# Optimization experiments

Hardware: AMD Instinct MI355X
Metric: run time of the kernel (lower is better)

## Reference

```python
import jax, jax.numpy as jnp
import numpy as np

N_NODES = 50000
N_EDGES = 800000
FEAT_SIZE = 4096
EMB = 30          # embedding_size
HID = 80          # hidden_size
VOCAB = 10
HEADS = 2
TEMP = 1.0
GAT_SLOPE = 0.2   # DGL GATConv leaky_relu negative_slope
CONV_SLOPE = 0.01 # torch LeakyReLU default


def _lrelu(x, s):
    return jnp.where(x >= 0, x, s * x)


def gat_layer(feat, W, al, ar, b, src, dst, n_nodes):
    """DGL GATConv: feat [N, ..., Fin] -> [N, ..., H, Fout].
    W: [Fin, H*Fout]; al, ar, b: [H, Fout]."""
    H, F = al.shape
    z = jnp.tensordot(feat, W, axes=1).reshape(feat.shape[:-1] + (H, F))  # [N,...,H,F]
    el = (z * al).sum(-1, keepdims=True)  # [N,...,H,1]
    er = (z * ar).sum(-1, keepdims=True)
    e = _lrelu(el[src] + er[dst], GAT_SLOPE)            # [E,...,H,1]
    emax = jax.ops.segment_max(e, dst, num_segments=n_nodes)
    ex = jnp.exp(e - emax[dst])
    denom = jax.ops.segment_sum(ex, dst, num_segments=n_nodes)
    alpha = ex / denom[dst]                              # edge softmax per dst
    rst = jax.ops.segment_sum(z[src] * alpha, dst, num_segments=n_nodes)
    return rst + b


def setup_inputs() -> dict:
    key = jax.random.key(0)
    ks = jax.random.split(key, 24)
    s = 0.1
    return {
        "x": jax.random.normal(ks[0], (2, FEAT_SIZE), jnp.float32),
        "vocab": jax.random.normal(ks[1], (VOCAB,), jnp.float32),
        "node_feats": jax.random.normal(ks[2], (2, N_NODES, 3), jnp.float32),
        "src": jax.random.randint(ks[3], (2, N_EDGES), 0, N_NODES, jnp.int32),
        "dst": jax.random.randint(ks[4], (2, N_EDGES), 0, N_NODES, jnp.int32),
        "W_lin1": jax.random.normal(ks[5], (FEAT_SIZE, EMB), jnp.float32) * s,
        "Wc1": jax.random.normal(ks[6], (HID, 2), jnp.float32) * s,
        "Wc2": jax.random.normal(ks[7], (HID,), jnp.float32) * s,
        "gat1_W": jax.random.normal(ks[8], (3, HEADS * HID), jnp.float32) * s,
        "gat1_al": jax.random.normal(ks[9], (HEADS, HID), jnp.float32) * s,
        "gat1_ar": jax.random.normal(ks[10], (HEADS, HID), jnp.float32) * s,
        "gat1_b": jax.random.normal(ks[11], (HEADS, HID), jnp.float32) * s,
        "gat2_W": jax.random.normal(ks[12], (HID, HEADS * EMB), jnp.float32) * s,
        "gat2_al": jax.random.normal(ks[13], (HEADS, EMB), jnp.float32) * s,
        "gat2_ar": jax.random.normal(ks[14], (HEADS, EMB), jnp.float32) * s,
        "gat2_b": jax.random.normal(ks[15], (HEADS, EMB), jnp.float32) * s,
        "Wg1": jax.random.normal(ks[16], (2 * EMB, EMB), jnp.float32) * s,
        "bg1": jax.random.normal(ks[17], (EMB,), jnp.float32) * s,
        "W2": jax.random.normal(ks[18], (2 * EMB + VOCAB, HID), jnp.float32) * s,
        "W3": jax.random.normal(ks[19], (HID, 2), jnp.float32) * s,
    }


def reference(x, vocab, node_feats, src, dst, W_lin1, Wc1, Wc2,
              gat1_W, gat1_al, gat1_ar, gat1_b,
              gat2_W, gat2_al, gat2_ar, gat2_b,
              Wg1, bg1, W2, W3):
    # deterministic order = [0, 1] (original shuffles); order.index(0) == 0
    # image branch: per-game embedding -> [2, EMB]
    emb = x @ W_lin1                          # [2, EMB]
    h = _lrelu(Wc1 @ emb, CONV_SLOPE)         # im_conv1: [HID, EMB]
    h = _lrelu(Wc2 @ h, CONV_SLOPE)           # im_conv2: [EMB]
    # graph branch: two GAT layers per graph, mean over nodes, take head 0
    gr_emb = []
    for i in range(2):
        g1 = gat_layer(node_feats[i], gat1_W, gat1_al, gat1_ar, gat1_b,
                       src[i], dst[i], N_NODES)          # [N, H, HID]
        g1 = jax.nn.relu(g1)
        g2 = gat_layer(g1, gat2_W, gat2_al, gat2_ar, gat2_b,
                       src[i], dst[i], N_NODES)          # [N, H, H, EMB]
        a = g2.mean(axis=0)[0, 0]                        # mean_nodes then a[0][0][0] -> [EMB]
        gr_emb.append(a)
    gr = jnp.concatenate(gr_emb) @ Wg1 + bg1             # [EMB]
    hc = jnp.concatenate([gr, h, vocab])                 # [2*EMB + VOCAB]
    logits = jax.nn.log_softmax(((hc @ W2) @ W3) * (1.0 / TEMP), axis=0)
    return logits, 0
```

## Files before the change

### kernel.cpp

```cpp
#include <hip/hip_runtime.h>
#include <math.h>

#define NN 50000
#define NE 800000

#define CH 196
#define C  256
#define CAP 3600
#define BSL 2048

__device__ __forceinline__ float lrelu(float x, float s) { return x >= 0.f ? x : s * x; }

__global__ void k_pre(const float* __restrict__ x, const float* __restrict__ Wl,
                      const float* __restrict__ nodef,
                      const float* __restrict__ W1, const float* __restrict__ al1,
                      const float* __restrict__ ar1,
                      const int* __restrict__ src, const int* __restrict__ dst,
                      float* __restrict__ imgp, float* __restrict__ feat4,
                      float* __restrict__ er1, unsigned* __restrict__ gctr,
                      unsigned* __restrict__ dbin, unsigned* __restrict__ sbin) {
    int bid = blockIdx.x, t = threadIdx.x;
    if (bid < 64) {
        __shared__ float part[8][64];
        int kk = t & 31, rq = t >> 5;
        int r0 = bid * 64;
        float a0 = 0.f, a1 = 0.f;
        if (kk < 30) {
            for (int i = 0; i < 8; ++i) {
                int r = r0 + rq * 8 + i;
                float wv = Wl[r * 30 + kk];
                a0 += x[r] * wv;
                a1 += x[4096 + r] * wv;
            }
        }
        part[rq][kk] = a0;
        part[rq][32 + kk] = a1;
        __syncthreads();
        if (t < 60) {
            int g = t / 30, k = t - g * 30;
            float s = 0.f;
            #pragma unroll
            for (int rr = 0; rr < 8; ++rr) s += part[rr][g * 32 + k];
            imgp[bid * 64 + g * 32 + k] = s;
        }
    } else if (bid < 456) {
        __shared__ float sP[6];
        if (t < 6) {
            int c = t >> 1;
            const float* av = (t & 1) ? ar1 : al1;
            float s = 0.f;
            for (int f = 0; f < 80; ++f) s += W1[c * 160 + f] * av[f];
            sP[(t & 1) * 3 + c] = s;
        }
        __syncthreads();
        int b2 = bid - 64;
        int g = b2 / 196;
        int n = (b2 - g * 196) * 256 + t;
        if (n < NN) {
            const float* f = nodef + ((size_t)g * NN + n) * 3;
            float f0 = f[0], f1 = f[1], f2 = f[2];
            *(float4*)(feat4 + ((size_t)g * NN + n) * 4) =
                make_float4(f0, f1, f2, f0 * sP[0] + f1 * sP[1] + f2 * sP[2]);
            er1[g * NN + n] = f0 * sP[3] + f1 * sP[4] + f2 * sP[5];
        }
    } else {
        __shared__ unsigned wcnt[4][C];
        __shared__ unsigned wbase[4][C];
        __shared__ unsigned wrun[4][C];
        __shared__ unsigned sbase2[C];
        int b3 = bid - 456;
        int a = b3 / 782;
        int rem2 = b3 - a * 782;
        int g = rem2 / 391;
        int bx = rem2 - g * 391;
        int wid = t >> 6;
        for (int i = t; i < 4 * C; i += 256) ((unsigned*)wcnt)[i] = 0;
        __syncthreads();
        const int* ip = (a ? src : dst) + (size_t)g * NE;
        const int* pp = (a ? dst : src) + (size_t)g * NE;
        unsigned* bin = (a ? sbin : dbin);
        int cbase = (a * 2 + g) * C;
        int bbase = g * C;
        int e0 = bx * BSL + t * 8;
        int nv = 0;
        if (e0 < NE) nv = (NE - e0) < 8 ? (NE - e0) : 8;
        unsigned cj[8], pk[8];
        if (nv == 8) {
            int4 v0 = *(const int4*)(ip + e0), v1 = *(const int4*)(ip + e0 + 4);
            int4 q0 = *(const int4*)(pp + e0), q1 = *(const int4*)(pp + e0 + 4);
            int dj[8] = {v0.x, v0.y, v0.z, v0.w, v1.x, v1.y, v1.z, v1.w};
            int pj[8] = {q0.x, q0.y, q0.z, q0.w, q1.x, q1.y, q1.z, q1.w};
            #pragma unroll
            for (int j = 0; j < 8; ++j) {
                unsigned c = (unsigned)dj[j] / CH;
                cj[j] = c;
                pk[j] = (((unsigned)dj[j] - c * CH) << 16) | (unsigned)pj[j];
                atomicAdd(&wcnt[wid][c], 1u);
            }
        } else {
            for (int j = 0; j < nv; ++j) {
                int dv = ip[e0 + j], pv = pp[e0 + j];
                unsigned c = (unsigned)dv / CH;
                cj[j] = c;
                pk[j] = (((unsigned)dv - c * CH) << 16) | (unsigned)pv;
                atomicAdd(&wcnt[wid][c], 1u);
            }
        }
        __syncthreads();
        if (t < C) {
            unsigned s = wcnt[0][t] + wcnt[1][t] + wcnt[2][t] + wcnt[3][t];
            sbase2[t] = atomicAdd(&gctr[cbase + t], s);
        }
        __syncthreads();
        for (int i = t; i < 4 * C; i += 256) {
            int w2 = i / C, b = i - w2 * C;
            unsigned off2 = 0;
            for (int w3 = 0; w3 < w2; ++w3) off2 += wcnt[w3][b];
            wbase[w2][b] = sbase2[b] + off2;
            wrun[w2][b] = 0;
        }
        __syncthreads();
        for (int j = 0; j < nv; ++j) {
            unsigned c = cj[j];
            unsigned slot = atomicAdd(&wrun[wid][c], 1u);
            unsigned pos = wbase[wid][c] + slot;
            if (pos < CAP) bin[(size_t)(bbase + c) * CAP + pos] = pk[j];
        }
    }
}

__global__ __launch_bounds__(1024) void k_e1n(const unsigned* __restrict__ dbin,
                                              const unsigned* __restrict__ gctr,
                                              const float* __restrict__ feat4,
                                              const float* __restrict__ er1,
                                              const float* __restrict__ W1,
                                              const float* __restrict__ b1,
                                              const float* __restrict__ W2,
                                              const float* __restrict__ al2,
                                              const float* __restrict__ ar2,
                                              float* __restrict__ facc4,
                                              float* __restrict__ el2,
                                              float* __restrict__ er2iv) {
    __shared__ unsigned scnt[CH];
    __shared__ unsigned sstart[CH + 1];
    __shared__ unsigned sofs[CH];
    __shared__ unsigned ssort[CAP];
    __shared__ float sEr[CH];
    __shared__ float pacc[8][CH];
    __shared__ float sW[240], sB[80], sU[80], sV[80];
    int c = blockIdx.x, g = blockIdx.y, t = threadIdx.x;
    int base = c * CH;
    if (t < CH) {
        scnt[t] = 0;
        sEr[t] = (base + t < NN) ? er1[(size_t)g * NN + base + t] : 0.f;
    }
    if (t >= 1024 - 80) {
        int f = t - (1024 - 80);
        sW[f] = W1[f];
        sW[80 + f] = W1[160 + f];
        sW[160 + f] = W1[320 + f];
        sB[f] = b1[f];
        float u = 0.f, v = 0.f;
        for (int j = 0; j < 30; ++j) {
            float wv = W2[f * 60 + j];
            u += wv * al2[j];
            v += wv * ar2[j];
        }
        sU[f] = u;
        sV[f] = v;
    }
    __syncthreads();
    const unsigned* seg = dbin + (size_t)(g * C + c) * CAP;
    unsigned size = gctr[g * C + c];
    if (size > CAP) size = CAP;
    for (unsigned i = t; i < size; i += 1024) atomicAdd(&scnt[seg[i] >> 16], 1u);
    __syncthreads();
    if (t == 0) {
        unsigned run = 0;
        for (int j = 0; j < CH; ++j) { sstart[j] = run; run += scnt[j]; }
        sstart[CH] = run;
    }
    __syncthreads();
    if (t < CH) sofs[t] = sstart[t];
    __syncthreads();
    for (unsigned i = t; i < size; i += 1024) {
        unsigned p = seg[i];
        unsigned slot = atomicAdd(&sofs[p >> 16], 1u);
        ssort[slot] = p & 0xFFFFu;
    }
    __syncthreads();
    const float* f4 = feat4 + (size_t)g * NN * 4;
    if (t < 2 * CH) {
        int rel = t >> 1, half = t & 1;
        unsigned start = sstart[rel], end = sstart[rel + 1];
        unsigned mid = (start + end) >> 1;
        unsigned lo = half ? mid : start;
        unsigned hi = half ? end : mid;
        float ax = 0.f, ay = 0.f, az = 0.f, aw = 0.f;
        float erv = sEr[rel];
        for (unsigned j = lo; j < hi; ++j) {
            unsigned s = ssort[j];
            float4 F = *(const float4*)(f4 + (size_t)s * 4);
            float wv = __expf(lrelu(F.w + erv, 0.2f));
            ax += wv * F.x; ay += wv * F.y; az += wv * F.z; aw += wv;
        }
        int hb = half * 4;
        pacc[hb + 0][rel] = ax;
        pacc[hb + 1][rel] = ay;
        pacc[hb + 2][rel] = az;
        pacc[hb + 3][rel] = aw;
    }
    __syncthreads();
    if (t < CH && base + t < NN) {
        size_t n = (size_t)g * NN + base + t;
        float fx = pacc[0][t] + pacc[4][t];
        float fy = pacc[1][t] + pacc[5][t];
        float fz = pacc[2][t] + pacc[6][t];
        float fw = pacc[3][t] + pacc[7][t];
        *(float4*)(facc4 + n * 4) = make_float4(fx, fy, fz, fw);
        float inv = fw != 0.f ? 1.f / fw : 0.f;
        float c0 = fx * inv, c1 = fy * inv, c2 = fz * inv;
        float el = 0.f, er = 0.f;
        #pragma unroll
        for (int f = 0; f < 80; ++f) {
            float gg = c0 * sW[f] + c1 * sW[80 + f] + c2 * sW[160 + f] + sB[f];
            gg = gg > 0.f ? gg : 0.f;
            el += gg * sU[f];
            er += gg * sV[f];
        }
        el2[n] = el;
        er2iv[n * 2] = er;
    }
}

__global__ __launch_bounds__(1024) void k_e2d(const unsigned* __restrict__ dbin,
                                              const unsigned* __restrict__ gctr,
                                              const float* __restrict__ el2,
                                              float* __restrict__ er2iv) {
    __shared__ float sden[CH], sEr2[CH];
    int c = blockIdx.x, g = blockIdx.y, t = threadIdx.x;
    int base = c * CH;
    if (t < CH) {
        sden[t] = 0.f;
        sEr2[t] = (base + t < NN) ? er2iv[((size_t)g * NN + base + t) * 2] : 0.f;
    }
    __syncthreads();
    const float* el = el2 + (size_t)g * NN;
    const unsigned* seg = dbin + (size_t)(g * C + c) * CAP;
    unsigned size = gctr[g * C + c];
    if (size > CAP) size = CAP;
    for (unsigned i = t; i < size; i += 1024) {
        unsigned p = seg[i];
        unsigned rel = p >> 16;
        atomicAdd(&sden[rel], __expf(lrelu(el[p & 0xFFFFu] + sEr2[rel], 0.2f)));
    }
    __syncthreads();
    if (t < CH && base + t < NN) {
        float s = sden[t];
        er2iv[((size_t)g * NN + base + t) * 2 + 1] = s != 0.f ? 1.f / s : 0.f;
    }
}

__global__ __launch_bounds__(1024) void k_e3q(const unsigned* __restrict__ sbin,
                                              const unsigned* __restrict__ gctr,
                                              const float* __restrict__ el2,
                                              const float* __restrict__ er2iv,
                                              const float* __restrict__ facc4,
                                              const float* __restrict__ W1,
                                              const float* __restrict__ b1,
                                              float* __restrict__ Apart) {
    __shared__ float sq[CH], sEl[CH];
    __shared__ float cx[CH], cy[CH], cz[CH];
    __shared__ float pacc2[12][80];
    __shared__ float sW[240], sB[80];
    int c = blockIdx.x, g = blockIdx.y, t = threadIdx.x;
    int base = c * CH;
    if (t < CH) {
        sq[t] = 0.f;
        sEl[t] = (base + t < NN) ? el2[(size_t)g * NN + base + t] : 0.f;
    }
    if (t >= 1024 - 80) {
        int f = t - (1024 - 80);
        sW[f] = W1[f];
        sW[80 + f] = W1[160 + f];
        sW[160 + f] = W1[320 + f];
        sB[f] = b1[f];
    }
    __syncthreads();
    const float* er = er2iv + (size_t)g * NN * 2;
    const unsigned* seg = sbin + (size_t)(g * C + c) * CAP;
    unsigned size = gctr[(2 + g) * C + c];
    if (size > CAP) size = CAP;
    for (unsigned i = t; i < size; i += 1024) {
        unsigned p = seg[i];
        unsigned rel = p >> 16;
        float2 E = *(const float2*)(er + 2 * (size_t)(p & 0xFFFFu));
        atomicAdd(&sq[rel], __expf(lrelu(sEl[rel] + E.x, 0.2f)) * E.y);
    }
    __syncthreads();
    if (t < CH) {
        if (base + t < NN) {
            float4 fa = *(const float4*)(facc4 + ((size_t)g * NN + base + t) * 4);
            float inv = fa.w != 0.f ? 1.f / fa.w : 0.f;
            cx[t] = fa.x * inv; cy[t] = fa.y * inv; cz[t] = fa.z * inv;
        } else {
            cx[t] = 0.f; cy[t] = 0.f; cz[t] = 0.f;
        }
    }
    __syncthreads();
    int grp = t / 80, f = t - grp * 80;
    if (grp < 12) {
        float acc = 0.f;
        float wf0 = sW[f], wf1 = sW[80 + f], wf2 = sW[160 + f], bf = sB[f];
        for (int i = grp; i < CH; i += 12) {
            float qn = sq[i];
            float gg = cx[i] * wf0 + cy[i] * wf1 + cz[i] * wf2 + bf;
            gg = gg > 0.f ? gg : 0.f;
            acc += qn * gg;
        }
        pacc2[grp][f] = acc;
    }
    __syncthreads();
    if (t < 80) {
        float s = 0.f;
        #pragma unroll
        for (int j = 0; j < 12; ++j) s += pacc2[j][t];
        Apart[((size_t)g * C + c) * 80 + t] = s;
    }
}

__global__ void k_final(const float* __restrict__ Apart, const float* __restrict__ imgp,
                        const float* __restrict__ W2g, const float* __restrict__ b2,
                        const float* __restrict__ Wg1, const float* __restrict__ bg1,
                        const float* __restrict__ Wc1, const float* __restrict__ Wc2,
                        const float* __restrict__ vocab, const float* __restrict__ W2f,
                        const float* __restrict__ W3, float* __restrict__ out, int out_size) {
    __shared__ float sA[160];
    __shared__ float emb[60];
    __shared__ float hh[80 * 30];
    __shared__ float a[60];
    __shared__ float hc[70];
    __shared__ float tt[80];
    __shared__ float lp[2];
    int t = threadIdx.x;
    if (t < 160) {
        int g = t / 80, f = t - g * 80;
        float s = 0.f;
        const float* Ap = Apart + (size_t)g * C * 80 + f;
        for (int c = 0; c < C; ++c) s += Ap[(size_t)c * 80];
        sA[t] = s;
    } else if (t < 220) {
        int q = t - 160;
        int g = q / 30, j = q - g * 30;
        float s = 0.f;
        for (int b = 0; b < 64; ++b) s += imgp[b * 64 + g * 32 + j];
        emb[q] = s;
    }
    __syncthreads();
    if (t < 60) {
        int i = t / 30, j = t % 30;
        float acc = 0.f;
        for (int f = 0; f < 80; ++f) acc += sA[i * 80 + f] * W2g[f * 60 + j];
        a[t] = acc * (1.f / NN) + b2[j];
    }
    __syncthreads();
    for (int p = t; p < 2400; p += 256) {
        int i = p / 30, j = p % 30;
        float v = Wc1[i * 2 + 0] * emb[j] + Wc1[i * 2 + 1] * emb[30 + j];
        hh[p] = lrelu(v, 0.01f);
    }
    __syncthreads();
    if (t < 30) {
        float acc = 0.f;
        for (int i = 0; i < 80; ++i) acc += Wc2[i] * hh[i * 30 + t];
        hc[30 + t] = lrelu(acc, 0.01f);
        float acg = bg1[t];
        for (int j = 0; j < 60; ++j) acg += a[j] * Wg1[j * 30 + t];
        hc[t] = acg;
        if (t < 10) hc[60 + t] = vocab[t];
    }
    __syncthreads();
    if (t < 80) {
        float acc = 0.f;
        for (int qd = 0; qd < 70; ++qd) acc += hc[qd] * W2f[qd * 80 + t];
        tt[t] = acc;
    }
    __syncthreads();
    if (t < 2) {
        float acc = 0.f;
        for (int p = 0; p < 80; ++p) acc += tt[p] * W3[p * 2 + t];
        lp[t] = acc;
    }
    __syncthreads();
    if (t == 0) {
        float m = fmaxf(lp[0], lp[1]);
        float lse = m + logf(expf(lp[0] - m) + expf(lp[1] - m));
        out[0] = lp[0] - lse;
        out[1] = lp[1] - lse;
    }
    for (int i = 2 + t; i < out_size; i += blockDim.x) out[i] = 0.f;
}

extern "C" void kernel_launch(void* const* d_in, const int* in_sizes, int n_in,
                              void* d_out, int out_size, void* d_ws, size_t ws_size,
                              hipStream_t stream) {
    const float* x        = (const float*)d_in[0];
    const float* vocab    = (const float*)d_in[1];
    const float* nodef    = (const float*)d_in[2];
    const int*   src      = (const int*)d_in[3];
    const int*   dst      = (const int*)d_in[4];
    const float* W_lin1   = (const float*)d_in[5];
    const float* Wc1      = (const float*)d_in[6];
    const float* Wc2      = (const float*)d_in[7];
    const float* gat1_W   = (const float*)d_in[8];
    const float* gat1_al  = (const float*)d_in[9];
    const float* gat1_ar  = (const float*)d_in[10];
    const float* gat1_b   = (const float*)d_in[11];
    const float* gat2_W   = (const float*)d_in[12];
    const float* gat2_al  = (const float*)d_in[13];
    const float* gat2_ar  = (const float*)d_in[14];
    const float* gat2_b   = (const float*)d_in[15];
    const float* Wg1      = (const float*)d_in[16];
    const float* bg1      = (const float*)d_in[17];
    const float* W2       = (const float*)d_in[18];
    const float* W3       = (const float*)d_in[19];
    (void)in_sizes; (void)n_in; (void)ws_size;

    float* w = (float*)d_ws;
    size_t off = 0;
    auto alloc = [&](size_t n) { size_t o = off; off += (n + 63) & ~(size_t)63; return o; };
    size_t o_ctr  = alloc(1024);
    size_t o_imgp = alloc(64 * 64);
    size_t o_Ap   = alloc((size_t)2 * C * 80);
    size_t o_feat = alloc((size_t)2 * NN * 4);
    size_t o_er1  = alloc(2 * NN);
    size_t o_el2  = alloc(2 * NN);
    size_t o_eriv = alloc((size_t)2 * NN * 2);
    size_t o_facc = alloc((size_t)2 * NN * 4);
    size_t o_dbin = alloc((size_t)2 * C * CAP);
    size_t o_sbin = alloc((size_t)2 * C * CAP);
    unsigned* gctr = (unsigned*)(w + o_ctr);
    unsigned* dbin = (unsigned*)(w + o_dbin);
    unsigned* sbin = (unsigned*)(w + o_sbin);

    hipMemsetAsync(w + o_ctr, 0, 1024 * sizeof(float), stream);
    k_pre<<<2020, 256, 0, stream>>>(x, W_lin1, nodef, gat1_W, gat1_al, gat1_ar,
                                    src, dst, w + o_imgp, w + o_feat, w + o_er1,
                                    gctr, dbin, sbin);

    k_e1n<<<dim3(C, 2), 1024, 0, stream>>>(dbin, gctr, w + o_feat, w + o_er1,
                                           gat1_W, gat1_b, gat2_W, gat2_al, gat2_ar,
                                           w + o_facc, w + o_el2, w + o_eriv);

    k_e2d<<<dim3(C, 2), 1024, 0, stream>>>(dbin, gctr, w + o_el2, w + o_eriv);

    k_e3q<<<dim3(C, 2), 1024, 0, stream>>>(sbin, gctr, w + o_el2, w + o_eriv,
                                           w + o_facc, gat1_W, gat1_b, w + o_Ap);

    k_final<<<1, 256, 0, stream>>>(w + o_Ap, w + o_imgp, gat2_W, gat2_b, Wg1, bg1,
                                   Wc1, Wc2, vocab, W2, W3, (float*)d_out, out_size);
}
```

Measured before the change: 100.8 us.

## Sort edges per block in LDS before scattering to bins with coalesced writes

The preprocessing kernel now runs 1024-thread blocks that each handle 8192 edges. Each block counting-sorts its packed edges by chunk in shared memory, then writes them out so consecutive threads store consecutive bin slots. This replaces the old scattered per-wave bin writes and cuts the number of global counter atomics by using fewer, larger blocks. The cost is an extra LDS pass and a serial prefix sum done by one thread. Edge order inside each bin stays nondeterministic, as before.

```diff
diff --git a/kernel.cpp b/kernel.cpp
--- a/kernel.cpp
+++ b/kernel.cpp
@@ -7,23 +7,24 @@
 #define CH 196
 #define C  256
 #define CAP 3600
-#define BSL 2048
+#define BSL 8192
 
 __device__ __forceinline__ float lrelu(float x, float s) { return x >= 0.f ? x : s * x; }
 
-__global__ void k_pre(const float* __restrict__ x, const float* __restrict__ Wl,
-                      const float* __restrict__ nodef,
-                      const float* __restrict__ W1, const float* __restrict__ al1,
-                      const float* __restrict__ ar1,
-                      const int* __restrict__ src, const int* __restrict__ dst,
-                      float* __restrict__ imgp, float* __restrict__ feat4,
-                      float* __restrict__ er1, unsigned* __restrict__ gctr,
-                      unsigned* __restrict__ dbin, unsigned* __restrict__ sbin) {
+__global__ __launch_bounds__(1024) void k_pre(
+        const float* __restrict__ x, const float* __restrict__ Wl,
+        const float* __restrict__ nodef,
+        const float* __restrict__ W1, const float* __restrict__ al1,
+        const float* __restrict__ ar1,
+        const int* __restrict__ src, const int* __restrict__ dst,
+        float* __restrict__ imgp, float* __restrict__ feat4,
+        float* __restrict__ er1, unsigned* __restrict__ gctr,
+        unsigned* __restrict__ dbin, unsigned* __restrict__ sbin) {
     int bid = blockIdx.x, t = threadIdx.x;
-    if (bid < 64) {
-        __shared__ float part[8][64];
+    if (bid < 16) {
+        __shared__ float part[32][64];
         int kk = t & 31, rq = t >> 5;
-        int r0 = bid * 64;
+        int r0 = bid * 256;
         float a0 = 0.f, a1 = 0.f;
         if (kk < 30) {
             for (int i = 0; i < 8; ++i) {
@@ -40,10 +41,10 @@
             int g = t / 30, k = t - g * 30;
             float s = 0.f;
             #pragma unroll
-            for (int rr = 0; rr < 8; ++rr) s += part[rr][g * 32 + k];
+            for (int rr = 0; rr < 32; ++rr) s += part[rr][g * 32 + k];
             imgp[bid * 64 + g * 32 + k] = s;
         }
-    } else if (bid < 456) {
+    } else if (bid < 114) {
         __shared__ float sP[6];
         if (t < 6) {
             int c = t >> 1;
@@ -53,28 +54,28 @@
             sP[(t & 1) * 3 + c] = s;
         }
         __syncthreads();
-        int b2 = bid - 64;
-        int g = b2 / 196;
-        int n = (b2 - g * 196) * 256 + t;
-        if (n < NN) {
-            const float* f = nodef + ((size_t)g * NN + n) * 3;
+        int flat = (bid - 16) * 1024 + t;
+        if (flat < 2 * NN) {
+            int g = flat / NN;
+            int n = flat - g * NN;
+            const float* f = nodef + (size_t)flat * 3;
             float f0 = f[0], f1 = f[1], f2 = f[2];
-            *(float4*)(feat4 + ((size_t)g * NN + n) * 4) =
+            *(float4*)(feat4 + (size_t)flat * 4) =
                 make_float4(f0, f1, f2, f0 * sP[0] + f1 * sP[1] + f2 * sP[2]);
             er1[g * NN + n] = f0 * sP[3] + f1 * sP[4] + f2 * sP[5];
         }
     } else {
-        __shared__ unsigned wcnt[4][C];
-        __shared__ unsigned wbase[4][C];
-        __shared__ unsigned wrun[4][C];
-        __shared__ unsigned sbase2[C];
-        int b3 = bid - 456;
-        int a = b3 / 782;
-        int rem2 = b3 - a * 782;
-        int g = rem2 / 391;
-        int bx = rem2 - g * 391;
-        int wid = t >> 6;
-        for (int i = t; i < 4 * C; i += 256) ((unsigned*)wcnt)[i] = 0;
+        __shared__ unsigned scnt[C];
+        __shared__ unsigned sstart[C + 1];
+        __shared__ unsigned sbase[C];
+        __shared__ unsigned sofs[C];
+        __shared__ unsigned ssort[BSL];
+        int b3 = bid - 114;
+        int a = b3 / 196;
+        int rem = b3 - a * 196;
+        int g = rem / 98;
+        int bx = rem - g * 98;
+        if (t < C) scnt[t] = 0;
         __syncthreads();
         const int* ip = (a ? src : dst) + (size_t)g * NE;
         const int* pp = (a ? dst : src) + (size_t)g * NE;
@@ -84,7 +85,7 @@
         int e0 = bx * BSL + t * 8;
         int nv = 0;
         if (e0 < NE) nv = (NE - e0) < 8 ? (NE - e0) : 8;
-        unsigned cj[8], pk[8];
+        unsigned pk[8];
         if (nv == 8) {
             int4 v0 = *(const int4*)(ip + e0), v1 = *(const int4*)(ip + e0 + 4);
             int4 q0 = *(const int4*)(pp + e0), q1 = *(const int4*)(pp + e0 + 4);
@@ -93,38 +94,41 @@
             #pragma unroll
             for (int j = 0; j < 8; ++j) {
                 unsigned c = (unsigned)dj[j] / CH;
-                cj[j] = c;
-                pk[j] = (((unsigned)dj[j] - c * CH) << 16) | (unsigned)pj[j];
-                atomicAdd(&wcnt[wid][c], 1u);
+                pk[j] = (c << 24) | (((unsigned)dj[j] - c * CH) << 16) | (unsigned)pj[j];
+                atomicAdd(&scnt[c], 1u);
             }
         } else {
             for (int j = 0; j < nv; ++j) {
                 int dv = ip[e0 + j], pv = pp[e0 + j];
                 unsigned c = (unsigned)dv / CH;
-                cj[j] = c;
-                pk[j] = (((unsigned)dv - c * CH) << 16) | (unsigned)pv;
-                atomicAdd(&wcnt[wid][c], 1u);
+                pk[j] = (c << 24) | (((unsigned)dv - c * CH) << 16) | (unsigned)pv;
+                atomicAdd(&scnt[c], 1u);
             }
         }
         __syncthreads();
+        if (t == 0) {
+            unsigned run = 0;
+            for (int j = 0; j < C; ++j) { sstart[j] = run; run += scnt[j]; }
+            sstart[C] = run;
+        }
+        __syncthreads();
         if (t < C) {
-            unsigned s = wcnt[0][t] + wcnt[1][t] + wcnt[2][t] + wcnt[3][t];
-            sbase2[t] = atomicAdd(&gctr[cbase + t], s);
-        }
-        __syncthreads();
-        for (int i = t; i < 4 * C; i += 256) {
-            int w2 = i / C, b = i - w2 * C;
-            unsigned off2 = 0;
-            for (int w3 = 0; w3 < w2; ++w3) off2 += wcnt[w3][b];
-            wbase[w2][b] = sbase2[b] + off2;
-            wrun[w2][b] = 0;
+            sbase[t] = atomicAdd(&gctr[cbase + t], scnt[t]);
+            sofs[t] = sstart[t];
         }
         __syncthreads();
         for (int j = 0; j < nv; ++j) {
-            unsigned c = cj[j];
-            unsigned slot = atomicAdd(&wrun[wid][c], 1u);
-            unsigned pos = wbase[wid][c] + slot;
-            if (pos < CAP) bin[(size_t)(bbase + c) * CAP + pos] = pk[j];
+            unsigned c = pk[j] >> 24;
+            unsigned slot = atomicAdd(&sofs[c], 1u);
+            ssort[slot] = pk[j];
+        }
+        __syncthreads();
+        unsigned total = sstart[C];
+        for (unsigned i = t; i < total; i += 1024) {
+            unsigned v = ssort[i];
+            unsigned c = v >> 24;
+            unsigned pos = sbase[c] + (i - sstart[c]);
+            if (pos < CAP) bin[(size_t)(bbase + c) * CAP + pos] = v & 0xFFFFFFu;
         }
     }
 }
@@ -353,7 +357,7 @@
         int q = t - 160;
         int g = q / 30, j = q - g * 30;
         float s = 0.f;
-        for (int b = 0; b < 64; ++b) s += imgp[b * 64 + g * 32 + j];
+        for (int b = 0; b < 16; ++b) s += imgp[b * 64 + g * 32 + j];
         emb[q] = s;
     }
     __syncthreads();
@@ -430,7 +434,7 @@
     size_t off = 0;
     auto alloc = [&](size_t n) { size_t o = off; off += (n + 63) & ~(size_t)63; return o; };
     size_t o_ctr  = alloc(1024);
-    size_t o_imgp = alloc(64 * 64);
+    size_t o_imgp = alloc(16 * 64);
     size_t o_Ap   = alloc((size_t)2 * C * 80);
     size_t o_feat = alloc((size_t)2 * NN * 4);
     size_t o_er1  = alloc(2 * NN);
@@ -444,7 +448,7 @@
     unsigned* sbin = (unsigned*)(w + o_sbin);
 
     hipMemsetAsync(w + o_ctr, 0, 1024 * sizeof(float), stream);
-    k_pre<<<2020, 256, 0, stream>>>(x, W_lin1, nodef, gat1_W, gat1_al, gat1_ar,
+    k_pre<<<506, 1024, 0, stream>>>(x, W_lin1, nodef, gat1_W, gat1_al, gat1_ar,
                                     src, dst, w + o_imgp, w + o_feat, w + o_er1,
                                     gctr, dbin, sbin);
 
```

After: 86.40 us, median of 2. 14.3% less time.
